# Kernel tuning notes

Hardware: AMD Instinct MI355X
Metric: run time of the kernel (lower is better)

Reference implementation:

```python
import jax, jax.numpy as jnp
import numpy as np

N = 65536          # number of macroscopic states (road cells)
Q = 512            # Q_mesoscale: velocity quadrature points
VMIN, VMAX = 0.0, 70.0
STOP = 1e-3        # stop_criterion used in forward()
MAX_ITER = 100


def setup_inputs() -> dict:
    key = jax.random.key(0)
    # macro velocities in the interior of [VMIN, VMAX] so Newton is well-conditioned
    macro_velocity = jax.random.uniform(key, (N, 1), dtype=jnp.float32,
                                        minval=5.0, maxval=65.0)
    xi = jnp.linspace(VMIN, VMAX, Q, dtype=jnp.float32)  # buffer self.xi
    return {"macro_velocity": macro_velocity, "xi": xi}


def _moments(lam, xi, xi2):
    # lam: [N,1], xi/xi2: [Q] -> E: [N,Q]
    E = jnp.exp(lam * xi[None, :])
    S0 = E.sum(axis=1, keepdims=True)
    S1 = (E * xi[None, :]).sum(axis=1, keepdims=True)
    S2 = (E * xi2[None, :]).sum(axis=1, keepdims=True)
    return S0, S1, S2


def _solve_lambda_mu(macro_velocity, xi):
    xi2 = xi * xi
    lam0 = jnp.zeros_like(macro_velocity)
    S0, S1, S2 = _moments(lam0, xi, xi2)
    gprime = (S0 * S2 - S1 * S1) / (S0 * S0)

    def cond(state):
        lam, S0, S1, S2, gp, c = state
        return (c < MAX_ITER) & (jnp.max(jnp.abs(gp)) > STOP)

    def body(state):
        lam, S0, S1, S2, gp, c = state
        lam1 = lam - (S1 / S0 - macro_velocity) / gp
        S0n, S1n, S2n = _moments(lam1, xi, xi2)
        gpn = (S0n * S2n - S1n * S1n) / (S0n * S0n)
        return (lam1, S0n, S1n, S2n, gpn, c + 1)

    lam, S0, _, _, _, _ = jax.lax.while_loop(
        cond, body, (lam0, S0, S1, S2, gprime, jnp.int32(0)))
    mu0 = -jnp.log(S0)
    return lam, mu0


def reference(macro_velocity, xi):
    lam, mu0 = _solve_lambda_mu(macro_velocity, xi)
    # f_eq = exp(mu0) * exp(lambda * xi)  -> [N, Q]
    return jnp.exp(mu0) * jnp.exp(lam * xi[None, :])
```

## Files before the change

kernel.cpp:

```cpp
#include <hip/hip_runtime.h>
#include <math.h>

#define N_CELLS 65536
#define Q_PTS   512
#define CPB     32
#define F4C     128
#define TPB     256


__global__ void __launch_bounds__(256)
fused_kernel(const float* __restrict__ u_in,
             const float4* __restrict__ xi4,
             float4* __restrict__ out4) {
    __shared__ float2 lm_s[CPB];
    const int t = threadIdx.x;

    const float4 x = xi4[t & 127];

    if (t < CPB) {
        const float DX = 70.0f / 511.0f;
        const float L  = 512.0f * 70.0f / 511.0f;
        const float V0 = (L * L - DX * DX) / 12.0f;
        const float C4_720 = (L*L*L*L - DX*DX*DX*DX) / 720.0f;
        const float C4_240 = (L*L*L*L - DX*DX*DX*DX) / 240.0f;
        const float A = L - 0.5f * DX - 35.0f;

        const float u = u_in[blockIdx.x * CPB + t];
        const float w = u - 35.0f;

        float lam;
        if (fabsf(w) < 15.0f) lam = w / V0;
        else                  lam = copysignf(1.0f / (A - fabsf(w)), w);

        #pragma unroll
        for (int it = 0; it < 4; ++it) {
            float m, v;
            if (fabsf(lam) > 1e-3f) {
                float gL = -1.0f / expm1f(-lam * L);
                float gd = -1.0f / expm1f(-lam * DX);
                m = L * gL - DX * gd;
                v = L * L * (gL - gL * gL) - DX * DX * (gd - gd * gd);
            } else {
                m = 35.0f + lam * (V0 - lam * lam * C4_720);
                v = V0 - lam * lam * C4_240;
            }
            lam -= (m - u) / v;
            lam = fminf(fmaxf(lam, -2.0f), 2.0f);
        }

        float logS0;
        if (fabsf(lam) > 1e-3f) {
            logS0 = logf(expm1f(lam * L) / expm1f(lam * DX));
        } else {
            logS0 = logf(512.0f) + lam * 35.0f + 0.5f * lam * lam * V0;
        }
        lm_s[t] = make_float2(lam, -logS0);
    }
    __syncthreads();

    const int base = blockIdx.x * (CPB * F4C);
    #pragma unroll
    for (int i = 0; i < (CPB * F4C) / TPB; ++i) {
        int idx = i * TPB + t;
        float2 p = lm_s[idx >> 7];
        float4 r;
        r.x = __expf(fmaf(p.x, x.x, p.y));
        r.y = __expf(fmaf(p.x, x.y, p.y));
        r.z = __expf(fmaf(p.x, x.z, p.y));
        r.w = __expf(fmaf(p.x, x.w, p.y));
        out4[base + idx] = r;
    }
}

extern "C" void kernel_launch(void* const* d_in, const int* in_sizes, int n_in,
                              void* d_out, int out_size, void* d_ws, size_t ws_size,
                              hipStream_t stream) {
    const float* macro_u = (const float*)d_in[0];
    const float* xi      = (const float*)d_in[1];
    float* out = (float*)d_out;

    fused_kernel<<<N_CELLS / CPB, TPB, 0, stream>>>(
        macro_u, (const float4*)xi, (float4*)out);
}
```

Before: 27.22 us.

## Solve Newton per wavefront and broadcast via readlane instead of shared memory

Each wavefront now solves for its own 8 cells, with lanes computing redundantly, and broadcasts lambda and mu through readlane. This removes the shared-memory staging and the block barrier, so the other waves no longer sit idle while 32 threads run Newton. It also drops the Newton loop from 4 to 3 iterations and pre-scales by log2(e) so the hardware exp2 can be used directly. The risks are somewhat less accurate lambda from one fewer iteration and redundant transcendental work in every lane.

New measurement: 26.49 us (median of 2 runs). 1.03x faster.

```diff
diff --git a/kernel.cpp b/kernel.cpp
--- a/kernel.cpp
+++ b/kernel.cpp
@@ -12,63 +12,66 @@
 fused_kernel(const float* __restrict__ u_in,
              const float4* __restrict__ xi4,
              float4* __restrict__ out4) {
-    __shared__ float2 lm_s[CPB];
-    const int t = threadIdx.x;
+    const int t  = threadIdx.x;
+    const int wv = t >> 6;
+    const int l  = t & 63;
 
-    const float4 x = xi4[t & 127];
+    const float4 x_lo = xi4[l];
+    const float4 x_hi = xi4[64 + l];
 
-    if (t < CPB) {
-        const float DX = 70.0f / 511.0f;
-        const float L  = 512.0f * 70.0f / 511.0f;
-        const float V0 = (L * L - DX * DX) / 12.0f;
-        const float C4_720 = (L*L*L*L - DX*DX*DX*DX) / 720.0f;
-        const float C4_240 = (L*L*L*L - DX*DX*DX*DX) / 240.0f;
-        const float A = L - 0.5f * DX - 35.0f;
+    const float u = u_in[blockIdx.x * CPB + wv * 8 + (l & 7)];
 
-        const float u = u_in[blockIdx.x * CPB + t];
-        const float w = u - 35.0f;
+    const float DX = 70.0f / 511.0f;
+    const float L  = 512.0f * 70.0f / 511.0f;
+    const float V0 = (L * L - DX * DX) / 12.0f;
+    const float C4_720 = (L*L*L*L - DX*DX*DX*DX) / 720.0f;
+    const float C4_240 = (L*L*L*L - DX*DX*DX*DX) / 240.0f;
+    const float A = L - 0.5f * DX - 35.0f;
+    const float LOG2E = 1.44269504088896340736f;
 
-        float lam;
-        if (fabsf(w) < 15.0f) lam = w / V0;
-        else                  lam = copysignf(1.0f / (A - fabsf(w)), w);
+    const float w = u - 35.0f;
+    float lam;
+    if (fabsf(w) < 15.0f) lam = w / V0;
+    else                  lam = copysignf(1.0f / (A - fabsf(w)), w);
 
-        #pragma unroll
-        for (int it = 0; it < 4; ++it) {
-            float m, v;
-            if (fabsf(lam) > 1e-3f) {
-                float gL = -1.0f / expm1f(-lam * L);
-                float gd = -1.0f / expm1f(-lam * DX);
-                m = L * gL - DX * gd;
-                v = L * L * (gL - gL * gL) - DX * DX * (gd - gd * gd);
-            } else {
-                m = 35.0f + lam * (V0 - lam * lam * C4_720);
-                v = V0 - lam * lam * C4_240;
-            }
-            lam -= (m - u) / v;
-            lam = fminf(fmaxf(lam, -2.0f), 2.0f);
+    #pragma unroll
+    for (int it = 0; it < 3; ++it) {
+        float m, v;
+        if (fabsf(lam) > 1e-3f) {
+            float gL = -1.0f / expm1f(-lam * L);
+            float gd = -1.0f / expm1f(-lam * DX);
+            m = L * gL - DX * gd;
+            v = L * L * (gL - gL * gL) - DX * DX * (gd - gd * gd);
+        } else {
+            m = 35.0f + lam * (V0 - lam * lam * C4_720);
+            v = V0 - lam * lam * C4_240;
         }
+        lam -= (m - u) / v;
+        lam = fminf(fmaxf(lam, -2.0f), 2.0f);
+    }
 
-        float logS0;
-        if (fabsf(lam) > 1e-3f) {
-            logS0 = logf(expm1f(lam * L) / expm1f(lam * DX));
-        } else {
-            logS0 = logf(512.0f) + lam * 35.0f + 0.5f * lam * lam * V0;
-        }
-        lm_s[t] = make_float2(lam, -logS0);
+    float logS0;
+    if (fabsf(lam) > 1e-3f) {
+        logS0 = logf(expm1f(lam * L) / expm1f(lam * DX));
+    } else {
+        logS0 = logf(512.0f) + lam * 35.0f + 0.5f * lam * lam * V0;
     }
-    __syncthreads();
 
-    const int base = blockIdx.x * (CPB * F4C);
+    const float lam2 = lam * LOG2E;
+    const float mu2  = -logS0 * LOG2E;
+
+    const int base = blockIdx.x * (CPB * F4C) + wv * (8 * F4C) + l;
     #pragma unroll
-    for (int i = 0; i < (CPB * F4C) / TPB; ++i) {
-        int idx = i * TPB + t;
-        float2 p = lm_s[idx >> 7];
+    for (int i = 0; i < 16; ++i) {
+        float a = __int_as_float(__builtin_amdgcn_readlane(__float_as_int(lam2), i >> 1));
+        float b = __int_as_float(__builtin_amdgcn_readlane(__float_as_int(mu2),  i >> 1));
+        float4 x = (i & 1) ? x_hi : x_lo;
         float4 r;
-        r.x = __expf(fmaf(p.x, x.x, p.y));
-        r.y = __expf(fmaf(p.x, x.y, p.y));
-        r.z = __expf(fmaf(p.x, x.z, p.y));
-        r.w = __expf(fmaf(p.x, x.w, p.y));
-        out4[base + idx] = r;
+        r.x = __builtin_amdgcn_exp2f(fmaf(a, x.x, b));
+        r.y = __builtin_amdgcn_exp2f(fmaf(a, x.y, b));
+        r.z = __builtin_amdgcn_exp2f(fmaf(a, x.z, b));
+        r.w = __builtin_amdgcn_exp2f(fmaf(a, x.w, b));
+        out4[base + i * 64] = r;
     }
 }
 
```
